# Optimization experiments

Hardware: AMD Instinct MI355X
Metric: run time of the kernel (lower is better)

Reference implementation:

```python
import jax, jax.numpy as jnp
import numpy as np

B = 1024
N_CPGS = 20000
N_FREQS = N_CPGS // 2 + 1  # 10001
HIDDEN = (256, 128, 64)
LN_EPS = 1e-5


def setup_inputs() -> dict:
    key = jax.random.key(0)
    keys = jax.random.split(key, 16)
    inp = {"x": jax.random.normal(keys[0], (B, N_CPGS), dtype=jnp.float32)}
    in_dim = N_FREQS
    for i, h in enumerate(HIDDEN):
        inp[f"W{i}"] = jax.random.normal(keys[1 + i], (h, in_dim), dtype=jnp.float32) * 0.01
        inp[f"alpha{i}"] = jnp.full((h, in_dim), 0.01, dtype=jnp.float32)
        inp[f"b{i}"] = jnp.zeros((h,), dtype=jnp.float32)
        inp[f"eta{i}"] = jnp.asarray(0.1, dtype=jnp.float32)
        inp[f"g{i}"] = jnp.ones((h,), dtype=jnp.float32)   # LayerNorm gamma
        inp[f"be{i}"] = jnp.zeros((h,), dtype=jnp.float32)  # LayerNorm beta
        in_dim = h
    inp["head_w"] = jax.random.normal(keys[10], (1, in_dim), dtype=jnp.float32) * (1.0 / np.sqrt(in_dim))
    inp["head_b"] = jnp.zeros((1,), dtype=jnp.float32)
    return inp


def _hebbian_layer(x, W, alpha, b, eta):
    # y_slow = x W^T + b;  plastic[b,i] = eta * tanh(y_slow)[b,i] * sum_j sigmoid(alpha)[i,j] * x_norm[b,j] * x[b,j]
    y_slow = jnp.einsum('bd,hd->bh', x, W) + b
    x_norm = x / (jnp.linalg.norm(x, axis=-1, keepdims=True) + 1e-8)
    c = x_norm * x  # (B, in) -- collapses the (B,out,in) outer-product trace algebraically
    plastic = eta * jnp.tanh(y_slow) * jnp.einsum('bd,hd->bh', c, jax.nn.sigmoid(alpha))
    return y_slow + plastic


def _layer_norm(h, g, be):
    mu = jnp.mean(h, axis=-1, keepdims=True)
    var = jnp.mean((h - mu) ** 2, axis=-1, keepdims=True)
    return (h - mu) * jax.lax.rsqrt(var + LN_EPS) * g + be


def reference(x, W0, alpha0, b0, eta0, g0, be0,
              W1, alpha1, b1, eta1, g1, be1,
              W2, alpha2, b2, eta2, g2, be2,
              head_w, head_b):
    # FFT spectral front-end
    xc = x - jnp.mean(x, axis=1, keepdims=True)
    h = jnp.log1p(jnp.abs(jnp.fft.rfft(xc, axis=1)))  # (B, N_FREQS)
    params = [(W0, alpha0, b0, eta0, g0, be0),
              (W1, alpha1, b1, eta1, g1, be1),
              (W2, alpha2, b2, eta2, g2, be2)]
    for (W, a, b, eta, g, be) in params:
        h = jax.nn.gelu(_layer_norm(_hebbian_layer(h, W, a, b, eta), g, be), approximate=False)
        # dropout is identity in eval mode
    return (jnp.einsum('bd,od->bo', h, head_w) + head_b)[:, 0]  # (B,)
```

## Files before the change

### kernel.cpp

```cpp
#include <hip/hip_runtime.h>
#include <hip/hip_bf16.h>
#include <math.h>

typedef short bf16x8 __attribute__((ext_vector_type(8)));
typedef float f32x4 __attribute__((ext_vector_type(4)));

static __device__ __forceinline__ unsigned short f2bf(float f) {
    unsigned int u = __float_as_uint(f);
    unsigned int r = (u + 0x7fffu + ((u >> 16) & 1u)) >> 16;
    return (unsigned short)r;
}

static __device__ __forceinline__ bf16x8 sq_bf16x8(bf16x8 a) {
    bf16x8 r;
    #pragma unroll
    for (int i = 0; i < 8; ++i) {
        unsigned int u = ((unsigned int)(unsigned short)a[i]) << 16;
        float f = __uint_as_float(u);
        f *= f;
        r[i] = (short)f2bf(f);
    }
    return r;
}

static __device__ __forceinline__ float gelu_f(float x) {
    return 0.5f * x * (1.f + erff(x * 0.70710678118654752f));
}

static __device__ __forceinline__ void gload_lds16(const void* g, void* l) {
    __builtin_amdgcn_global_load_lds(
        (const __attribute__((address_space(1))) unsigned int*)g,
        (__attribute__((address_space(3))) unsigned int*)l, 16, 0, 0);
}

static __device__ __forceinline__ int ldsmap(int i) { return i + (i >> 6); }

static __device__ __forceinline__ int rev4(int k) {
    int d0 = k % 10; k /= 10;
    int d1 = k % 10; k /= 10;
    int d2 = k % 10; int d3 = k / 10;
    return d0 * 1000 + d1 * 100 + d2 * 10 + d3;
}

static __device__ __forceinline__ void dft5(
    float a0r, float a0i, float a1r, float a1i, float a2r, float a2i,
    float a3r, float a3i, float a4r, float a4i,
    float* Xr, float* Xi)
{
    const float c1 = 0.30901699437494742f, c2 = -0.80901699437494745f;
    const float s1 = 0.95105651629515357f, s2 = 0.58778525229247312f;
    float t1r = a1r + a4r, t1i = a1i + a4i;
    float d1r = a1r - a4r, d1i = a1i - a4i;
    float t2r = a2r + a3r, t2i = a2i + a3i;
    float d2r = a2r - a3r, d2i = a2i - a3i;
    Xr[0] = a0r + t1r + t2r; Xi[0] = a0i + t1i + t2i;
    float m1r = a0r + c1 * t1r + c2 * t2r, m1i = a0i + c1 * t1i + c2 * t2i;
    float m2r = a0r + c2 * t1r + c1 * t2r, m2i = a0i + c2 * t1i + c1 * t2i;
    float n1r = s1 * d1r + s2 * d2r, n1i = s1 * d1i + s2 * d2i;
    float n2r = s2 * d1r - s1 * d2r, n2i = s2 * d1i - s1 * d2i;
    Xr[1] = m1r + n1i; Xi[1] = m1i - n1r;
    Xr[4] = m1r - n1i; Xi[4] = m1i + n1r;
    Xr[2] = m2r + n2i; Xi[2] = m2i - n2r;
    Xr[3] = m2r - n2i; Xi[3] = m2i + n2r;
}

template<int S>
static __device__ __forceinline__ void radix10_core(
    float* __restrict__ reb, float* __restrict__ imb,
    const float* ar, const float* ai, int base, int j)
{
    constexpr int L  = (S == 0) ? 1000 : (S == 1) ? 100 : (S == 2) ? 10 : 1;
    constexpr int SC = (S == 0) ? 1 : (S == 1) ? 10 : (S == 2) ? 100 : 1000;
    constexpr bool TW = (S != 3);

    const float WR[5] = {1.f, 0.80901699437494745f, 0.30901699437494742f,
                         -0.30901699437494742f, -0.80901699437494745f};
    const float WI[5] = {0.f, -0.58778525229247312f, -0.95105651629515357f,
                         -0.95105651629515357f, -0.58778525229247312f};

    float Er[5], Ei[5], Or[5], Oi[5];
    dft5(ar[0], ai[0], ar[2], ai[2], ar[4], ai[4], ar[6], ai[6], ar[8], ai[8], Er, Ei);
    dft5(ar[1], ai[1], ar[3], ai[3], ar[5], ai[5], ar[7], ai[7], ar[9], ai[9], Or, Oi);
    #pragma unroll
    for (int k = 1; k < 5; ++k) {
        float tr = Or[k] * WR[k] - Oi[k] * WI[k];
        Oi[k] = Or[k] * WI[k] + Oi[k] * WR[k];
        Or[k] = tr;
    }

    if (TW) {
        const float ang = (float)(j * SC) * -6.28318530717958648e-4f;
        float w1c, w1s;
        __sincosf(ang, &w1s, &w1c);
        float twr[10], twi[10];
        twr[0] = 1.f; twi[0] = 0.f;
        #pragma unroll
        for (int t = 1; t < 10; ++t) {
            twr[t] = twr[t - 1] * w1c - twi[t - 1] * w1s;
            twi[t] = twr[t - 1] * w1s + twi[t - 1] * w1c;
        }
        #pragma unroll
        for (int k = 0; k < 5; ++k) {
            float xr0 = Er[k] + Or[k], xi0 = Ei[k] + Oi[k];
            float xr1 = Er[k] - Or[k], xi1 = Ei[k] - Oi[k];
            int i0 = ldsmap(base + k * L);
            int i1 = ldsmap(base + (k + 5) * L);
            if (k == 0) {
                reb[i0] = xr0;
                imb[i0] = xi0;
            } else {
                reb[i0] = xr0 * twr[k] - xi0 * twi[k];
                imb[i0] = xr0 * twi[k] + xi0 * twr[k];
            }
            reb[i1] = xr1 * twr[k + 5] - xi1 * twi[k + 5];
            imb[i1] = xr1 * twi[k + 5] + xi1 * twr[k + 5];
        }
    } else {
        #pragma unroll
        for (int k = 0; k < 5; ++k) {
            int i0 = ldsmap(base + k * L);
            int i1 = ldsmap(base + (k + 5) * L);
            reb[i0] = Er[k] + Or[k]; imb[i0] = Ei[k] + Oi[k];
            reb[i1] = Er[k] - Or[k]; imb[i1] = Ei[k] - Oi[k];
        }
    }
}

template<int S>
static __device__ __forceinline__ void radix10_stage(
    float* __restrict__ reb, float* __restrict__ imb, int tid)
{
    constexpr int L = (S == 1) ? 100 : (S == 2) ? 10 : 1;
    for (int w = tid; w < 1000; w += 512) {
        int g, j;
        if (S == 3) { g = w; j = 0; }
        else        { g = w / L; j = w - g * L; }
        const int base = g * (10 * L) + j;
        float ar[10], ai[10];
        #pragma unroll
        for (int u = 0; u < 10; ++u) {
            int idx = ldsmap(base + u * L);
            ar[u] = reb[idx];
            ai[u] = imb[idx];
        }
        radix10_core<S>(reb, imb, ar, ai, base, j);
    }
}

__global__ __launch_bounds__(512, 4)
void fft_prep_kernel(const float* __restrict__ x,
                     unsigned short* __restrict__ hb,
                     float* __restrict__ hnorm,
                     const float* __restrict__ W0, const float* __restrict__ A0,
                     unsigned short* __restrict__ Wb, unsigned short* __restrict__ Sb,
                     const float* __restrict__ W1, const float* __restrict__ A1,
                     const float* __restrict__ W2, const float* __restrict__ A2,
                     float* __restrict__ W1T, float* __restrict__ S1T,
                     float* __restrict__ W2T, float* __restrict__ S2T)
{
    if (blockIdx.x >= 1024) {
        int idx = (blockIdx.x - 1024) * 512 + threadIdx.x;
        if (idx < 1280128) {
            const bool isW = idx < 640064;
            const int f4 = isW ? idx : idx - 640064;
            const float* src = isW ? W0 : A0;
            unsigned short* dst = isW ? Wb : Sb;
            float4 v = ((const float4*)src)[f4];
            float e[4] = {v.x, v.y, v.z, v.w};
            int flat = f4 * 4;
            int row = flat / 10001;
            int col = flat - row * 10001;
            #pragma unroll
            for (int i = 0; i < 4; ++i) {
                if (col == 10001) { row++; col = 0; }
                float val = isW ? e[i] : 1.f / (1.f + expf(-e[i]));
                dst[(size_t)row * 10240 + col] = f2bf(val);
                col++;
            }
        } else if (idx < 1341312) {
            int i = idx - 1280128;
            int row = i / 239;
            int col = 10001 + (i - row * 239);
            Wb[(size_t)row * 10240 + col] = 0;
            Sb[(size_t)row * 10240 + col] = 0;
        } else if (idx < 1423232) {
            int o = idx - 1341312;
            if (o < 32768) {
                int d = o >> 7, h = o & 127;
                W1T[o] = W1[h * 256 + d];
            } else if (o < 65536) {
                int p = o - 32768;
                int d = p >> 7, h = p & 127;
                S1T[p] = 1.f / (1.f + expf(-A1[h * 256 + d]));
            } else if (o < 73728) {
                int p = o - 65536;
                int d = p >> 6, h = p & 63;
                W2T[p] = W2[h * 128 + d];
            } else {
                int p = o - 73728;
                int d = p >> 6, h = p & 63;
                S2T[p] = 1.f / (1.f + expf(-A2[h * 128 + d]));
            }
        }
        return;
    }

    __shared__ float reb[10156];
    __shared__ float imb[10156];
    __shared__ float redbuf[8];

    const int b = blockIdx.x;
    const int tid = threadIdx.x;
    const int lane = tid & 63;
    const int wv = tid >> 6;

    const float2* z2 = (const float2*)(x + (size_t)b * 20000);
    for (int w = tid; w < 1000; w += 512) {
        float ar[10], ai[10];
        #pragma unroll
        for (int u = 0; u < 10; ++u) {
            float2 v = z2[w + u * 1000];
            ar[u] = v.x; ai[u] = v.y;
        }
        radix10_core<0>(reb, imb, ar, ai, w, w);
    }
    __syncthreads();
    radix10_stage<1>(reb, imb, tid);
    __syncthreads();
    radix10_stage<2>(reb, imb, tid);
    __syncthreads();
    radix10_stage<3>(reb, imb, tid);
    __syncthreads();

    float sumsq = 0.f;
    unsigned short* hrow = hb + (size_t)b * 10240;
    #pragma unroll
    for (int i = 0; i < 20; ++i) {
        int k = tid + i * 512;
        float hval = 0.f;
        if (k > 0 && k <= 10000) {
            int k1 = (k == 10000) ? 0 : k;
            int k2 = (k1 == 0) ? 0 : 10000 - k1;
            int i1 = ldsmap(rev4(k1));
            int i2 = ldsmap(rev4(k2));
            float zr = reb[i1], zi = imb[i1];
            float wr = reb[i2], wi = imb[i2];
            float er = 0.5f * (zr + wr);
            float ei = 0.5f * (zi - wi);
            float odr = 0.5f * (zi + wi);
            float odi = -0.5f * (zr - wr);
            float ct, st;
            __sincosf((float)k * -3.14159265358979324e-4f, &st, &ct);
            float xre = er + ct * odr - st * odi;
            float xim = ei + ct * odi + st * odr;
            hval = __logf(1.f + sqrtf(xre * xre + xim * xim));
        }
        hrow[k] = f2bf(hval);
        sumsq += hval * hval;
    }
    #pragma unroll
    for (int o = 32; o; o >>= 1) sumsq += __shfl_xor(sumsq, o);
    __syncthreads();
    if (lane == 0) redbuf[wv] = sumsq;
    __syncthreads();
    if (tid == 0) {
        float tsq = 0.f;
        #pragma unroll
        for (int i = 0; i < 8; ++i) tsq += redbuf[i];
        hnorm[b] = 1.f / (sqrtf(tsq) + 1e-8f);
    }
}

__global__ __launch_bounds__(256, 2)
void gemm0_kernel(const unsigned short* __restrict__ hb,
                  const unsigned short* __restrict__ Wb, const unsigned short* __restrict__ Sb,
                  float* __restrict__ Py, float* __restrict__ Pp)
{
    __shared__ unsigned short Ah[128 * 64];
    __shared__ unsigned short Bw[64 * 64];
    __shared__ unsigned short Bs[64 * 64];

    const int t = threadIdx.x;
    const int b0 = blockIdx.x * 128;
    const int n0 = blockIdx.y * 64;
    const int z = blockIdx.z;
    const int lane = t & 63;
    const int wv = t >> 6;
    const int ml = lane & 15;
    const int q4 = lane >> 4;
    const int s0 = q4 ^ (ml & 7);

    const int sub = lane >> 3;
    const int sl = lane & 7;
    const int gsw = sl ^ sub;

    f32x4 accY[2][4], accP[2][4];
    #pragma unroll
    for (int mt = 0; mt < 2; ++mt)
        #pragma unroll
        for (int nt = 0; nt < 4; ++nt) {
            accY[mt][nt] = (f32x4){0.f, 0.f, 0.f, 0.f};
            accP[mt][nt] = (f32x4){0.f, 0.f, 0.f, 0.f};
        }

    const int kbase = z * 640;

    for (int step = 0; step < 10; ++step) {
        const int k0 = kbase + step * 64;
        __syncthreads();
        #pragma unroll
        for (int j = 0; j < 4; ++j) {
            const int c = wv * 4 + j;
            const size_t go = (size_t)(b0 + c * 8 + sub) * 10240 + k0 + gsw * 8;
            gload_lds16(&hb[go], &Ah[c * 512]);
        }
        #pragma unroll
        for (int j = 0; j < 2; ++j) {
            const int c = wv * 2 + j;
            const size_t go = (size_t)(n0 + c * 8 + sub) * 10240 + k0 + gsw * 8;
            gload_lds16(&Wb[go], &Bw[c * 512]);
            gload_lds16(&Sb[go], &Bs[c * 512]);
        }
        __syncthreads();

        #pragma unroll
        for (int kk = 0; kk < 2; ++kk) {
            const int slot = (s0 ^ (kk << 2)) << 3;
            bf16x8 ah[2], ac[2], bw[4], bs[4];
            #pragma unroll
            for (int mt = 0; mt < 2; ++mt) {
                int mrow = wv * 32 + mt * 16 + ml;
                ah[mt] = *(const bf16x8*)&Ah[mrow * 64 + slot];
                ac[mt] = sq_bf16x8(ah[mt]);
            }
            #pragma unroll
            for (int nt = 0; nt < 4; ++nt) {
                int nrow = nt * 16 + ml;
                bw[nt] = *(const bf16x8*)&Bw[nrow * 64 + slot];
                bs[nt] = *(const bf16x8*)&Bs[nrow * 64 + slot];
            }
            #pragma unroll
            for (int mt = 0; mt < 2; ++mt)
                #pragma unroll
                for (int nt = 0; nt < 4; ++nt) {
                    accY[mt][nt] = __builtin_amdgcn_mfma_f32_16x16x32_bf16(ah[mt], bw[nt], accY[mt][nt], 0, 0, 0);
                    accP[mt][nt] = __builtin_amdgcn_mfma_f32_16x16x32_bf16(ac[mt], bs[nt], accP[mt][nt], 0, 0, 0);
                }
        }
    }

    const int rq = q4 * 4;
    #pragma unroll
    for (int mt = 0; mt < 2; ++mt)
        #pragma unroll
        for (int nt = 0; nt < 4; ++nt)
            #pragma unroll
            for (int r = 0; r < 4; ++r) {
                int m = b0 + wv * 32 + mt * 16 + rq + r;
                int n = n0 + nt * 16 + ml;
                size_t o = ((size_t)z * 1024 + m) * 256 + n;
                Py[o] = accY[mt][nt][r];
                Pp[o] = accP[mt][nt][r];
            }
}

__global__ __launch_bounds__(256)
void combine_tail_kernel(const float* __restrict__ Py, const float* __restrict__ Pp,
                 const float* __restrict__ hnorm,
                 const float* __restrict__ b0v, const float* __restrict__ eta0p,
                 const float* __restrict__ g0, const float* __restrict__ be0,
                 const float* __restrict__ W1T, const float* __restrict__ S1T,
                 const float* __restrict__ b1, const float* __restrict__ eta1p,
                 const float* __restrict__ g1, const float* __restrict__ be1,
                 const float* __restrict__ W2T, const float* __restrict__ S2T,
                 const float* __restrict__ b2, const float* __restrict__ eta2p,
                 const float* __restrict__ g2, const float* __restrict__ be2,
                 const float* __restrict__ hw, const float* __restrict__ hbod,
                 float* __restrict__ out)
{
    __shared__ float sh[4][256];
    __shared__ float sc[4][256];
    __shared__ float sv[4][128];
    __shared__ float sh2[4][128];
    __shared__ float sc2[4][128];
    __shared__ float sv2[4][64];
    __shared__ float redA[4][4];
    __shared__ float redB[4][4];

    const int t = threadIdx.x;
    const int b0 = blockIdx.x * 4;
    const int lane = t & 63;
    const int wv = t >> 6;

    const float e0 = eta0p[0];
    const float bias0 = b0v[t];
    float v[4];
    #pragma unroll
    for (int r = 0; r < 4; ++r) {
        float ys = 0.f, ps = 0.f;
        #pragma unroll 4
        for (int s = 0; s < 16; ++s) {
            size_t o = ((size_t)s * 1024 + b0 + r) * 256 + t;
            ys += Py[o];
            ps += Pp[o];
        }
        ps *= hnorm[b0 + r];
        float y = ys + bias0;
        v[r] = y + e0 * tanhf(y) * ps;
    }

    float s1[4], s2[4];
    #pragma unroll
    for (int r = 0; r < 4; ++r) { s1[r] = v[r]; s2[r] = v[r] * v[r]; }
    #pragma unroll
    for (int o = 32; o; o >>= 1)
        #pragma unroll
        for (int r = 0; r < 4; ++r) { s1[r] += __shfl_xor(s1[r], o); s2[r] += __shfl_xor(s2[r], o); }
    if (lane == 0)
        #pragma unroll
        for (int r = 0; r < 4; ++r) { redA[wv][r] = s1[r]; redB[wv][r] = s2[r]; }
    __syncthreads();

    const float gg = g0[t], bb = be0[t];
    float gl[4], s3[4];
    #pragma unroll
    for (int r = 0; r < 4; ++r) {
        float sum = redA[0][r] + redA[1][r] + redA[2][r] + redA[3][r];
        float sumsq = redB[0][r] + redB[1][r] + redB[2][r] + redB[3][r];
        float mu = sum * (1.f / 256.f);
        float var = sumsq * (1.f / 256.f) - mu * mu;
        float u = (v[r] - mu) * rsqrtf(var + 1e-5f) * gg + bb;
        gl[r] = gelu_f(u);
        s3[r] = gl[r] * gl[r];
    }
    #pragma unroll
    for (int o = 32; o; o >>= 1)
        #pragma unroll
        for (int r = 0; r < 4; ++r) s3[r] += __shfl_xor(s3[r], o);
    __syncthreads();
    if (lane == 0)
        #pragma unroll
        for (int r = 0; r < 4; ++r) redA[wv][r] = s3[r];
    __syncthreads();
    #pragma unroll
    for (int r = 0; r < 4; ++r) {
        float gsq = redA[0][r] + redA[1][r] + redA[2][r] + redA[3][r];
        float inv = 1.f / (sqrtf(gsq) + 1e-8f);
        sh[r][t] = gl[r];
        sc[r][t] = gl[r] * gl[r] * inv;
    }
    __syncthreads();

    const int hcol = t & 127;
    const int r2 = t >> 7;
    float ya[2] = {0.f, 0.f};
    float pa[2] = {0.f, 0.f};
    for (int d = 0; d < 256; ++d) {
        float w = W1T[d * 128 + hcol];
        float s = S1T[d * 128 + hcol];
        #pragma unroll
        for (int i = 0; i < 2; ++i) {
            int r = r2 * 2 + i;
            ya[i] += sh[r][d] * w;
            pa[i] += sc[r][d] * s;
        }
    }
    const float e1 = eta1p[0];
    #pragma unroll
    for (int i = 0; i < 2; ++i) {
        int r = r2 * 2 + i;
        float y = ya[i] + b1[hcol];
        sv[r][hcol] = y + e1 * tanhf(y) * pa[i];
    }
    __syncthreads();

    {
        int r = wv;
        float v0 = sv[r][lane];
        float v1 = sv[r][lane + 64];
        float s = v0 + v1, sq = v0 * v0 + v1 * v1;
        #pragma unroll
        for (int o = 32; o; o >>= 1) { s += __shfl_xor(s, o); sq += __shfl_xor(sq, o); }
        float mu = s * (1.f / 128.f);
        float var = sq * (1.f / 128.f) - mu * mu;
        float rs = rsqrtf(var + 1e-5f);
        float u0 = (v0 - mu) * rs * g1[lane] + be1[lane];
        float u1 = (v1 - mu) * rs * g1[lane + 64] + be1[lane + 64];
        float ge0 = gelu_f(u0);
        float ge1 = gelu_f(u1);
        float gsq = ge0 * ge0 + ge1 * ge1;
        #pragma unroll
        for (int o = 32; o; o >>= 1) gsq += __shfl_xor(gsq, o);
        float inv = 1.f / (sqrtf(gsq) + 1e-8f);
        sh2[r][lane] = ge0; sh2[r][lane + 64] = ge1;
        sc2[r][lane] = ge0 * ge0 * inv; sc2[r][lane + 64] = ge1 * ge1 * inv;
    }
    __syncthreads();

    const int h2c = t & 63;
    const int r4 = t >> 6;
    float yb = 0.f, pb = 0.f;
    for (int d = 0; d < 128; ++d) {
        yb += sh2[r4][d] * W2T[d * 64 + h2c];
        pb += sc2[r4][d] * S2T[d * 64 + h2c];
    }
    {
        const float e2 = eta2p[0];
        float y = yb + b2[h2c];
        sv2[r4][h2c] = y + e2 * tanhf(y) * pb;
    }
    __syncthreads();

    {
        int r = wv;
        float v0 = sv2[r][lane];
        float s = v0, sq = v0 * v0;
        #pragma unroll
        for (int o = 32; o; o >>= 1) { s += __shfl_xor(s, o); sq += __shfl_xor(sq, o); }
        float mu = s * (1.f / 64.f);
        float var = sq * (1.f / 64.f) - mu * mu;
        float rs = rsqrtf(var + 1e-5f);
        float u = (v0 - mu) * rs * g2[lane] + be2[lane];
        float g = gelu_f(u);
        float hc = g * hw[lane];
        #pragma unroll
        for (int o = 32; o; o >>= 1) hc += __shfl_xor(hc, o);
        if (lane == 0) out[b0 + r] = hc + hbod[0];
    }
}

extern "C" void kernel_launch(void* const* d_in, const int* in_sizes, int n_in,
                              void* d_out, int out_size, void* d_ws, size_t ws_size,
                              hipStream_t stream)
{
    const float* x    = (const float*)d_in[0];
    const float* W0   = (const float*)d_in[1];
    const float* A0   = (const float*)d_in[2];
    const float* b0   = (const float*)d_in[3];
    const float* eta0 = (const float*)d_in[4];
    const float* g0   = (const float*)d_in[5];
    const float* be0  = (const float*)d_in[6];
    const float* W1   = (const float*)d_in[7];
    const float* A1   = (const float*)d_in[8];
    const float* b1   = (const float*)d_in[9];
    const float* eta1 = (const float*)d_in[10];
    const float* g1   = (const float*)d_in[11];
    const float* be1  = (const float*)d_in[12];
    const float* W2   = (const float*)d_in[13];
    const float* A2   = (const float*)d_in[14];
    const float* b2   = (const float*)d_in[15];
    const float* eta2 = (const float*)d_in[16];
    const float* g2   = (const float*)d_in[17];
    const float* be2  = (const float*)d_in[18];
    const float* hw   = (const float*)d_in[19];
    const float* hbod = (const float*)d_in[20];
    float* out = (float*)d_out;

    char* w = (char*)d_ws;
    unsigned short* hb  = (unsigned short*)(w + 0);
    unsigned short* Wb0 = (unsigned short*)(w + 20971520);
    unsigned short* Sb0 = (unsigned short*)(w + 26214400);
    float* Py   = (float*)(w + 31457280);
    float* Pp   = (float*)(w + 48234496);
    float* W1T  = (float*)(w + 65011712);
    float* S1T  = (float*)(w + 65142784);
    float* W2T  = (float*)(w + 65273856);
    float* S2T  = (float*)(w + 65306624);
    float* hnm  = (float*)(w + 65339392);

    hipLaunchKernelGGL(fft_prep_kernel, dim3(3804), dim3(512), 0, stream,
                       x, hb, hnm, W0, A0, Wb0, Sb0, W1, A1, W2, A2, W1T, S1T, W2T, S2T);
    hipLaunchKernelGGL(gemm0_kernel, dim3(8, 4, 16), dim3(256), 0, stream, hb, Wb0, Sb0, Py, Pp);
    hipLaunchKernelGGL(combine_tail_kernel, dim3(256), dim3(256), 0, stream, Py, Pp, hnm,
                       b0, eta0, g0, be0, W1T, S1T, b1, eta1, g1, be1,
                       W2T, S2T, b2, eta2, g2, be2, hw, hbod, out);
}
```

Measured before the change: 252.6 us.

## Use precomputed FFT tables, XCD-aware GEMM mapping, and finer tail blocks

Adds an init kernel that precomputes the bit-reversal index pairs and twiddle factors, so the FFT reads them from global tables instead of computing sincos and digit reversal per element. The final pass now advances its twiddle with a rotation recurrence. The GEMM grid is flattened to 1D with an XCD-aware remap of split-K slices and occupancy is raised to 3. The tail kernel now handles 2 rows per block instead of 4, and the second layer's reduction is split across all threads. The extra launch and the global table reads add some cost, and the rotation recurrence may lose a little accuracy.

```diff
diff --git a/kernel.cpp b/kernel.cpp
--- a/kernel.cpp
+++ b/kernel.cpp
@@ -40,6 +40,25 @@
     int d1 = k % 10; k /= 10;
     int d2 = k % 10; int d3 = k / 10;
     return d0 * 1000 + d1 * 100 + d2 * 10 + d3;
+}
+
+__global__ __launch_bounds__(256)
+void init_tables_kernel(unsigned int* __restrict__ idxTab, float2* __restrict__ twTab)
+{
+    int i = blockIdx.x * 256 + threadIdx.x;
+    if (i < 10001) {
+        int k1 = (i == 10000) ? 0 : i;
+        int k2 = (k1 == 0) ? 0 : 10000 - k1;
+        unsigned a = (unsigned)ldsmap(rev4(k1));
+        unsigned b = (unsigned)ldsmap(rev4(k2));
+        idxTab[i] = a | (b << 16);
+    }
+    if (i < 8992) {
+        float ang = (float)i * -6.28318530717958648e-4f;
+        float s, c;
+        __sincosf(ang, &s, &c);
+        twTab[i] = make_float2(c, s);
+    }
 }
 
 static __device__ __forceinline__ void dft5(
@@ -67,7 +86,8 @@
 template<int S>
 static __device__ __forceinline__ void radix10_core(
     float* __restrict__ reb, float* __restrict__ imb,
-    const float* ar, const float* ai, int base, int j)
+    const float* ar, const float* ai, int base, int j,
+    const float2* __restrict__ twTab)
 {
     constexpr int L  = (S == 0) ? 1000 : (S == 1) ? 100 : (S == 2) ? 10 : 1;
     constexpr int SC = (S == 0) ? 1 : (S == 1) ? 10 : (S == 2) ? 100 : 1000;
@@ -89,15 +109,12 @@
     }
 
     if (TW) {
-        const float ang = (float)(j * SC) * -6.28318530717958648e-4f;
-        float w1c, w1s;
-        __sincosf(ang, &w1s, &w1c);
+        const int js = j * SC;
         float twr[10], twi[10];
-        twr[0] = 1.f; twi[0] = 0.f;
         #pragma unroll
         for (int t = 1; t < 10; ++t) {
-            twr[t] = twr[t - 1] * w1c - twi[t - 1] * w1s;
-            twi[t] = twr[t - 1] * w1s + twi[t - 1] * w1c;
+            float2 wv_ = twTab[js * t];
+            twr[t] = wv_.x; twi[t] = wv_.y;
         }
         #pragma unroll
         for (int k = 0; k < 5; ++k) {
@@ -128,7 +145,8 @@
 
 template<int S>
 static __device__ __forceinline__ void radix10_stage(
-    float* __restrict__ reb, float* __restrict__ imb, int tid)
+    float* __restrict__ reb, float* __restrict__ imb, int tid,
+    const float2* __restrict__ twTab)
 {
     constexpr int L = (S == 1) ? 100 : (S == 2) ? 10 : 1;
     for (int w = tid; w < 1000; w += 512) {
@@ -143,7 +161,7 @@
             ar[u] = reb[idx];
             ai[u] = imb[idx];
         }
-        radix10_core<S>(reb, imb, ar, ai, base, j);
+        radix10_core<S>(reb, imb, ar, ai, base, j, twTab);
     }
 }
 
@@ -156,7 +174,9 @@
                      const float* __restrict__ W1, const float* __restrict__ A1,
                      const float* __restrict__ W2, const float* __restrict__ A2,
                      float* __restrict__ W1T, float* __restrict__ S1T,
-                     float* __restrict__ W2T, float* __restrict__ S2T)
+                     float* __restrict__ W2T, float* __restrict__ S2T,
+                     const unsigned int* __restrict__ idxTab,
+                     const float2* __restrict__ twTab)
 {
     if (blockIdx.x >= 1024) {
         int idx = (blockIdx.x - 1024) * 512 + threadIdx.x;
@@ -222,16 +242,20 @@
             float2 v = z2[w + u * 1000];
             ar[u] = v.x; ai[u] = v.y;
         }
-        radix10_core<0>(reb, imb, ar, ai, w, w);
-    }
-    __syncthreads();
-    radix10_stage<1>(reb, imb, tid);
-    __syncthreads();
-    radix10_stage<2>(reb, imb, tid);
-    __syncthreads();
-    radix10_stage<3>(reb, imb, tid);
-    __syncthreads();
-
+        radix10_core<0>(reb, imb, ar, ai, w, w, twTab);
+    }
+    __syncthreads();
+    radix10_stage<1>(reb, imb, tid, twTab);
+    __syncthreads();
+    radix10_stage<2>(reb, imb, tid, twTab);
+    __syncthreads();
+    radix10_stage<3>(reb, imb, tid, twTab);
+    __syncthreads();
+
+    float ct, st;
+    __sincosf((float)tid * -3.14159265358979324e-4f, &st, &ct);
+    const float RC = 0.987091579f;
+    const float RS = -0.160156842f;
     float sumsq = 0.f;
     unsigned short* hrow = hb + (size_t)b * 10240;
     #pragma unroll
@@ -239,24 +263,24 @@
         int k = tid + i * 512;
         float hval = 0.f;
         if (k > 0 && k <= 10000) {
-            int k1 = (k == 10000) ? 0 : k;
-            int k2 = (k1 == 0) ? 0 : 10000 - k1;
-            int i1 = ldsmap(rev4(k1));
-            int i2 = ldsmap(rev4(k2));
+            unsigned pp = idxTab[k];
+            int i1 = (int)(pp & 0xffffu);
+            int i2 = (int)(pp >> 16);
             float zr = reb[i1], zi = imb[i1];
             float wr = reb[i2], wi = imb[i2];
             float er = 0.5f * (zr + wr);
             float ei = 0.5f * (zi - wi);
             float odr = 0.5f * (zi + wi);
             float odi = -0.5f * (zr - wr);
-            float ct, st;
-            __sincosf((float)k * -3.14159265358979324e-4f, &st, &ct);
             float xre = er + ct * odr - st * odi;
             float xim = ei + ct * odi + st * odr;
             hval = __logf(1.f + sqrtf(xre * xre + xim * xim));
         }
         hrow[k] = f2bf(hval);
         sumsq += hval * hval;
+        float nct = ct * RC - st * RS;
+        st = ct * RS + st * RC;
+        ct = nct;
     }
     #pragma unroll
     for (int o = 32; o; o >>= 1) sumsq += __shfl_xor(sumsq, o);
@@ -271,7 +295,7 @@
     }
 }
 
-__global__ __launch_bounds__(256, 2)
+__global__ __launch_bounds__(256, 3)
 void gemm0_kernel(const unsigned short* __restrict__ hb,
                   const unsigned short* __restrict__ Wb, const unsigned short* __restrict__ Sb,
                   float* __restrict__ Py, float* __restrict__ Pp)
@@ -281,18 +305,23 @@
     __shared__ unsigned short Bs[64 * 64];
 
     const int t = threadIdx.x;
-    const int b0 = blockIdx.x * 128;
-    const int n0 = blockIdx.y * 64;
-    const int z = blockIdx.z;
+    const int lin = blockIdx.x;
+    const int xcd = lin & 7;
+    const int sub = lin >> 3;
+    const int z = xcd * 2 + (sub & 1);
+    const int tile = sub >> 1;
+    const int b0 = (tile & 7) * 128;
+    const int n0 = (tile >> 3) * 64;
+
     const int lane = t & 63;
     const int wv = t >> 6;
     const int ml = lane & 15;
     const int q4 = lane >> 4;
     const int s0 = q4 ^ (ml & 7);
 
-    const int sub = lane >> 3;
+    const int sub8 = lane >> 3;
     const int sl = lane & 7;
-    const int gsw = sl ^ sub;
+    const int gsw = sl ^ sub8;
 
     f32x4 accY[2][4], accP[2][4];
     #pragma unroll
@@ -311,13 +340,13 @@
         #pragma unroll
         for (int j = 0; j < 4; ++j) {
             const int c = wv * 4 + j;
-            const size_t go = (size_t)(b0 + c * 8 + sub) * 10240 + k0 + gsw * 8;
+            const size_t go = (size_t)(b0 + c * 8 + sub8) * 10240 + k0 + gsw * 8;
             gload_lds16(&hb[go], &Ah[c * 512]);
         }
         #pragma unroll
         for (int j = 0; j < 2; ++j) {
             const int c = wv * 2 + j;
-            const size_t go = (size_t)(n0 + c * 8 + sub) * 10240 + k0 + gsw * 8;
+            const size_t go = (size_t)(n0 + c * 8 + sub8) * 10240 + k0 + gsw * 8;
             gload_lds16(&Wb[go], &Bw[c * 512]);
             gload_lds16(&Sb[go], &Bs[c * 512]);
         }
@@ -378,53 +407,57 @@
                  const float* __restrict__ hw, const float* __restrict__ hbod,
                  float* __restrict__ out)
 {
-    __shared__ float sh[4][256];
-    __shared__ float sc[4][256];
-    __shared__ float sv[4][128];
-    __shared__ float sh2[4][128];
-    __shared__ float sc2[4][128];
-    __shared__ float sv2[4][64];
-    __shared__ float redA[4][4];
-    __shared__ float redB[4][4];
+    __shared__ float sh[2][256];
+    __shared__ float sc[2][256];
+    __shared__ float sv[2][128];
+    __shared__ float sh2[2][128];
+    __shared__ float sc2[2][128];
+    __shared__ float sv2[2][64];
+    __shared__ float p2a[2][2][64];
+    __shared__ float p2b[2][2][64];
+    __shared__ float redA[4][2];
+    __shared__ float redB[4][2];
 
     const int t = threadIdx.x;
-    const int b0 = blockIdx.x * 4;
+    const int b0 = blockIdx.x * 2;
     const int lane = t & 63;
     const int wv = t >> 6;
 
     const float e0 = eta0p[0];
     const float bias0 = b0v[t];
-    float v[4];
-    #pragma unroll
-    for (int r = 0; r < 4; ++r) {
-        float ys = 0.f, ps = 0.f;
-        #pragma unroll 4
-        for (int s = 0; s < 16; ++s) {
+    float ys[2] = {0.f, 0.f}, ps[2] = {0.f, 0.f};
+    #pragma unroll 4
+    for (int s = 0; s < 16; ++s)
+        #pragma unroll
+        for (int r = 0; r < 2; ++r) {
             size_t o = ((size_t)s * 1024 + b0 + r) * 256 + t;
-            ys += Py[o];
-            ps += Pp[o];
-        }
-        ps *= hnorm[b0 + r];
-        float y = ys + bias0;
-        v[r] = y + e0 * tanhf(y) * ps;
-    }
-
-    float s1[4], s2[4];
-    #pragma unroll
-    for (int r = 0; r < 4; ++r) { s1[r] = v[r]; s2[r] = v[r] * v[r]; }
+            ys[r] += Py[o];
+            ps[r] += Pp[o];
+        }
+    float v[2];
+    #pragma unroll
+    for (int r = 0; r < 2; ++r) {
+        float p = ps[r] * hnorm[b0 + r];
+        float y = ys[r] + bias0;
+        v[r] = y + e0 * tanhf(y) * p;
+    }
+
+    float s1[2], s2[2];
+    #pragma unroll
+    for (int r = 0; r < 2; ++r) { s1[r] = v[r]; s2[r] = v[r] * v[r]; }
     #pragma unroll
     for (int o = 32; o; o >>= 1)
         #pragma unroll
-        for (int r = 0; r < 4; ++r) { s1[r] += __shfl_xor(s1[r], o); s2[r] += __shfl_xor(s2[r], o); }
+        for (int r = 0; r < 2; ++r) { s1[r] += __shfl_xor(s1[r], o); s2[r] += __shfl_xor(s2[r], o); }
     if (lane == 0)
         #pragma unroll
-        for (int r = 0; r < 4; ++r) { redA[wv][r] = s1[r]; redB[wv][r] = s2[r]; }
+        for (int r = 0; r < 2; ++r) { redA[wv][r] = s1[r]; redB[wv][r] = s2[r]; }
     __syncthreads();
 
     const float gg = g0[t], bb = be0[t];
-    float gl[4], s3[4];
-    #pragma unroll
-    for (int r = 0; r < 4; ++r) {
+    float gl[2], s3[2];
+    #pragma unroll
+    for (int r = 0; r < 2; ++r) {
         float sum = redA[0][r] + redA[1][r] + redA[2][r] + redA[3][r];
         float sumsq = redB[0][r] + redB[1][r] + redB[2][r] + redB[3][r];
         float mu = sum * (1.f / 256.f);
@@ -436,14 +469,14 @@
     #pragma unroll
     for (int o = 32; o; o >>= 1)
         #pragma unroll
-        for (int r = 0; r < 4; ++r) s3[r] += __shfl_xor(s3[r], o);
+        for (int r = 0; r < 2; ++r) s3[r] += __shfl_xor(s3[r], o);
     __syncthreads();
     if (lane == 0)
         #pragma unroll
-        for (int r = 0; r < 4; ++r) redA[wv][r] = s3[r];
-    __syncthreads();
-    #pragma unroll
-    for (int r = 0; r < 4; ++r) {
+        for (int r = 0; r < 2; ++r) redA[wv][r] = s3[r];
+    __syncthreads();
+    #pragma unroll
+    for (int r = 0; r < 2; ++r) {
         float gsq = redA[0][r] + redA[1][r] + redA[2][r] + redA[3][r];
         float inv = 1.f / (sqrtf(gsq) + 1e-8f);
         sh[r][t] = gl[r];
@@ -452,29 +485,21 @@
     __syncthreads();
 
     const int hcol = t & 127;
-    const int r2 = t >> 7;
-    float ya[2] = {0.f, 0.f};
-    float pa[2] = {0.f, 0.f};
+    const int r1 = t >> 7;
+    float ya = 0.f, pa = 0.f;
+    #pragma unroll 8
     for (int d = 0; d < 256; ++d) {
-        float w = W1T[d * 128 + hcol];
-        float s = S1T[d * 128 + hcol];
-        #pragma unroll
-        for (int i = 0; i < 2; ++i) {
-            int r = r2 * 2 + i;
-            ya[i] += sh[r][d] * w;
-            pa[i] += sc[r][d] * s;
-        }
-    }
-    const float e1 = eta1p[0];
-    #pragma unroll
-    for (int i = 0; i < 2; ++i) {
-        int r = r2 * 2 + i;
-        float y = ya[i] + b1[hcol];
-        sv[r][hcol] = y + e1 * tanhf(y) * pa[i];
-    }
-    __syncthreads();
-
+        ya += sh[r1][d] * W1T[d * 128 + hcol];
+        pa += sc[r1][d] * S1T[d * 128 + hcol];
+    }
     {
+        const float e1 = eta1p[0];
+        float y = ya + b1[hcol];
+        sv[r1][hcol] = y + e1 * tanhf(y) * pa;
+    }
+    __syncthreads();
+
+    if (wv < 2) {
         int r = wv;
         float v0 = sv[r][lane];
         float v1 = sv[r][lane + 64];
@@ -497,21 +522,33 @@
     }
     __syncthreads();
 
-    const int h2c = t & 63;
-    const int r4 = t >> 6;
-    float yb = 0.f, pb = 0.f;
-    for (int d = 0; d < 128; ++d) {
-        yb += sh2[r4][d] * W2T[d * 64 + h2c];
-        pb += sc2[r4][d] * S2T[d * 64 + h2c];
-    }
     {
+        const int h2c = t & 63;
+        const int r = (t >> 6) & 1;
+        const int dh = t >> 7;
+        float yb = 0.f, pb = 0.f;
+        #pragma unroll 8
+        for (int dd = 0; dd < 64; ++dd) {
+            int d = dh * 64 + dd;
+            yb += sh2[r][d] * W2T[d * 64 + h2c];
+            pb += sc2[r][d] * S2T[d * 64 + h2c];
+        }
+        p2a[dh][r][h2c] = yb;
+        p2b[dh][r][h2c] = pb;
+    }
+    __syncthreads();
+    if (t < 128) {
+        const int h2c = t & 63;
+        const int r = t >> 6;
         const float e2 = eta2p[0];
+        float yb = p2a[0][r][h2c] + p2a[1][r][h2c];
+        float pb = p2b[0][r][h2c] + p2b[1][r][h2c];
         float y = yb + b2[h2c];
-        sv2[r4][h2c] = y + e2 * tanhf(y) * pb;
-    }
-    __syncthreads();
-
-    {
+        sv2[r][h2c] = y + e2 * tanhf(y) * pb;
+    }
+    __syncthreads();
+
+    if (wv < 2) {
         int r = wv;
         float v0 = sv2[r][lane];
         float s = v0, sq = v0 * v0;
@@ -567,11 +604,15 @@
     float* W2T  = (float*)(w + 65273856);
     float* S2T  = (float*)(w + 65306624);
     float* hnm  = (float*)(w + 65339392);
-
+    unsigned int* idxT = (unsigned int*)(w + 65343488);
+    float2* twT = (float2*)(w + 65384448);
+
+    hipLaunchKernelGGL(init_tables_kernel, dim3(40), dim3(256), 0, stream, idxT, twT);
     hipLaunchKernelGGL(fft_prep_kernel, dim3(3804), dim3(512), 0, stream,
-                       x, hb, hnm, W0, A0, Wb0, Sb0, W1, A1, W2, A2, W1T, S1T, W2T, S2T);
-    hipLaunchKernelGGL(gemm0_kernel, dim3(8, 4, 16), dim3(256), 0, stream, hb, Wb0, Sb0, Py, Pp);
-    hipLaunchKernelGGL(combine_tail_kernel, dim3(256), dim3(256), 0, stream, Py, Pp, hnm,
+                       x, hb, hnm, W0, A0, Wb0, Sb0, W1, A1, W2, A2, W1T, S1T, W2T, S2T,
+                       idxT, twT);
+    hipLaunchKernelGGL(gemm0_kernel, dim3(512), dim3(256), 0, stream, hb, Wb0, Sb0, Py, Pp);
+    hipLaunchKernelGGL(combine_tail_kernel, dim3(512), dim3(256), 0, stream, Py, Pp, hnm,
                        b0, eta0, g0, be0, W1T, S1T, b1, eta1, g1, be1,
                        W2T, S2T, b2, eta2, g2, be2, hw, hbod, out);
 }
```

New measurement: 265.8 us. 1.05x slower.
